# Optimization experiments

Hardware: AMD Instinct MI355X
Metric: run time of the kernel (lower is better)

Reference implementation:

```python
import jax, jax.numpy as jnp
import numpy as np

N, E, R = 50000, 500000, 3
IN, HID, OUT = 128, 128, 128
NEG_SLOPE = 0.2


def setup_inputs() -> dict:
    key = jax.random.key(0)
    ks = jax.random.split(key, 16)
    g = lambda i, shape: jax.random.normal(ks[i], shape, jnp.float32) * 0.1
    return {
        "x": jax.random.normal(ks[0], (N, IN), jnp.float32),
        "edge_index": jax.random.randint(ks[1], (2, E), 0, N, jnp.int32),
        "edge_type": jax.random.randint(ks[2], (E,), 0, R, jnp.int32),
        "edge_attr": jax.random.normal(ks[3], (E, 1), jnp.float32),
        # conv1 params (RGATConv: per-relation weight, q/k/e attention vectors, edge lin, bias)
        "w1": g(4, (R, IN, HID)), "q1": g(5, (HID, 1)), "k1": g(6, (HID, 1)),
        "le1": g(7, (1, HID)), "e1": g(8, (HID, 1)), "b1": jnp.zeros((HID,), jnp.float32),
        # conv2 params
        "w2": g(9, (R, HID, OUT)), "q2": g(10, (OUT, 1)), "k2": g(11, (OUT, 1)),
        "le2": g(12, (1, OUT)), "e2": g(13, (OUT, 1)), "b2": jnp.zeros((OUT,), jnp.float32),
    }


def _rgat_conv(x, src, dst, edge_type, edge_attr, w, q, k, le, e, b):
    """PyG RGATConv: heads=1, dim=1, additive-self-attention, across-relation softmax."""
    n = x.shape[0]
    # Per-relation linear at node level (equiv. to per-edge bmm with w[edge_type])
    xw = jnp.einsum('ni,rio->rno', x, w)            # [R, N, C]
    x_j = xw[edge_type, src]                          # [E, C] transformed source feats
    x_i = xw[edge_type, dst]                          # [E, C] transformed target feats
    # additive attention logits: q(x_i) + k(x_j) + e(lin_edge(edge_attr))
    alpha = x_i @ q + x_j @ k + (edge_attr @ le) @ e  # [E, 1]
    alpha = jax.nn.leaky_relu(alpha, negative_slope=NEG_SLOPE)
    # across-relation softmax over incoming edges of each target node
    amax = jax.ops.segment_max(alpha, dst, num_segments=n)
    amax = jnp.where(jnp.isfinite(amax), amax, 0.0)   # empty segments -> 0
    ex = jnp.exp(alpha - amax[dst])
    denom = jax.ops.segment_sum(ex, dst, num_segments=n)
    alpha = ex / (denom[dst] + 1e-16)
    # weighted scatter-add aggregation, then bias (concat=True, heads=1)
    out = jax.ops.segment_sum(alpha * x_j, dst, num_segments=n)  # [N, C]
    return out + b


def reference(x, edge_index, edge_type, edge_attr,
              w1, q1, k1, le1, e1, b1,
              w2, q2, k2, le2, e2, b2):
    src, dst = edge_index[0], edge_index[1]
    h = jax.nn.relu(_rgat_conv(x, src, dst, edge_type, edge_attr, w1, q1, k1, le1, e1, b1))
    return _rgat_conv(h, src, dst, edge_type, edge_attr, w2, q2, k2, le2, e2, b2)
```

## Files before the change

kernel.cpp:

```cpp
#include <hip/hip_runtime.h>
#include <hip/hip_bf16.h>
#include <math.h>

typedef __bf16 bf16x8 __attribute__((ext_vector_type(8)));
typedef float f32x4 __attribute__((ext_vector_type(4)));

#define CDIM 128

__global__ void sentinel_kernel(float* outf) {
  if (threadIdx.x == 0) outf[0] = 12345.0f;
}

__global__ __launch_bounds__(256) void prep_hist_kernel(
    const float* __restrict__ w1, const float* __restrict__ w2,
    __hip_bfloat16* __restrict__ wt,
    const float* __restrict__ le1, const float* __restrict__ e1,
    const float* __restrict__ le2, const float* __restrict__ e2,
    float* __restrict__ outc, const int* __restrict__ dstv,
    int* __restrict__ deg, int perW, int E) {
  const int b = blockIdx.x;
  const int tid = threadIdx.x;
  if (b < 48) {
    int t = b * 256 + tid;
    if (t >= perW * 2) return;
    const float* w = (t < perW) ? w1 : w2;
    int tt = (t < perW) ? t : t - perW;
    int r = tt >> 11;
    int rem = tt & 2047;
    int kb = rem >> 7;
    int o = rem & 127;
    const float* wr = w + ((size_t)r << 14);
    union { __hip_bfloat16 h[8]; int4 v; } u;
#pragma unroll
    for (int j = 0; j < 8; ++j)
      u.h[j] = __float2bfloat16(wr[(size_t)(kb * 8 + j) * CDIM + o]);
    *reinterpret_cast<int4*>(wt + (size_t)t * 8) = u.v;
  } else if (b == 48) {
    if (tid < 64) {
      float v1 = le1[tid] * e1[tid] + le1[tid + 64] * e1[tid + 64];
      float v2 = le2[tid] * e2[tid] + le2[tid + 64] * e2[tid + 64];
#pragma unroll
      for (int off = 32; off > 0; off >>= 1) {
        v1 += __shfl_xor(v1, off, 64);
        v2 += __shfl_xor(v2, off, 64);
      }
      if (tid == 0) { outc[0] = v1; outc[1] = v2; }
    }
  } else {
    int e = (b - 49) * 256 + tid;
    if (e < E) atomicAdd(&deg[dstv[e]], 1);
  }
}


__global__ __launch_bounds__(256) void scan1_kernel(const int* __restrict__ deg,
                                                    int* __restrict__ rowptr,
                                                    int* __restrict__ partials, int n) {
  __shared__ int sh[256];
  int t = threadIdx.x;
  int base = blockIdx.x * 1024;
  int idx = base + t * 4;
  int v[4]; int s = 0;
#pragma unroll
  for (int j = 0; j < 4; ++j) { v[j] = (idx + j < n) ? deg[idx + j] : 0; s += v[j]; }
  sh[t] = s;
  __syncthreads();
  for (int off = 1; off < 256; off <<= 1) {
    int x = (t >= off) ? sh[t - off] : 0;
    __syncthreads();
    sh[t] += x;
    __syncthreads();
  }
  int excl = sh[t] - s;
  if (t == 255) partials[blockIdx.x] = sh[255];
  int run = excl;
#pragma unroll
  for (int j = 0; j < 4; ++j) {
    if (idx + j < n) rowptr[idx + j] = run;
    run += v[j];
  }
}

__global__ __launch_bounds__(256) void scan3_kernel(int* __restrict__ rowptr,
                                                    int* __restrict__ cursor,
                                                    const int* __restrict__ partials,
                                                    int nb, int n, int E) {
  __shared__ int spfx[64];
  int t = threadIdx.x;
  if (t < 64) {
    int pv = (t < nb) ? partials[t] : 0;
    int v = pv;
#pragma unroll
    for (int off = 1; off < 64; off <<= 1) {
      int u = __shfl_up(v, off, 64);
      if (t >= off) v += u;
    }
    spfx[t] = v - pv;
  }
  __syncthreads();
  int i = blockIdx.x * 256 + t;
  if (i < n) {
    int v = rowptr[i] + spfx[i >> 10];
    rowptr[i] = v;
    cursor[i] = v;
  } else if (i == n) {
    rowptr[n] = E;
  }
}

__device__ __forceinline__ void gemm_body(
    int tileb, const float* __restrict__ xin, const __hip_bfloat16* __restrict__ wt,
    const float* __restrict__ qv, const float* __restrict__ kv,
    __hip_bfloat16* __restrict__ xwout, float* __restrict__ sq,
    float* __restrict__ sk, int n, __hip_bfloat16* wlds, float* qls, float* kls) {
  const int base = tileb * 128;
  const int tid = threadIdx.x;
  const int wave = tid >> 6, lane = tid & 63;
  const int quad = lane >> 4, c16 = lane & 15;

  if (tid < 128) qls[tid] = qv[tid];
  else kls[tid - 128] = kv[tid - 128];

  bf16x8 zf;
#pragma unroll
  for (int j = 0; j < 8; ++j) zf[j] = (__bf16)0.0f;

  bf16x8 af[2][4];
#pragma unroll
  for (int h = 0; h < 2; ++h) {
    int m = base + wave * 32 + h * 16 + c16;
#pragma unroll
    for (int ks = 0; ks < 4; ++ks) {
      if (m < n) {
        const float* xp = xin + (size_t)m * CDIM + ks * 32 + quad * 8;
        f32x4 x0 = *reinterpret_cast<const f32x4*>(xp);
        f32x4 x1 = *reinterpret_cast<const f32x4*>(xp + 4);
        bf16x8 a;
#pragma unroll
        for (int j = 0; j < 4; ++j) { a[j] = (__bf16)x0[j]; a[4 + j] = (__bf16)x1[j]; }
        af[h][ks] = a;
      } else {
        af[h][ks] = zf;
      }
    }
  }

  for (int r = 0; r < 3; ++r) {
    if (r) __syncthreads();
    {
      const int4* src = reinterpret_cast<const int4*>(wt + ((size_t)r << 14));
      int4* dst = reinterpret_cast<int4*>(wlds);
#pragma unroll
      for (int i = 0; i < 8; ++i) dst[tid + i * 256] = src[tid + i * 256];
    }
    __syncthreads();

    f32x4 acc[2][8];
#pragma unroll
    for (int h = 0; h < 2; ++h)
#pragma unroll
      for (int ot = 0; ot < 8; ++ot) acc[h][ot] = (f32x4){0.f, 0.f, 0.f, 0.f};

#pragma unroll
    for (int ks = 0; ks < 4; ++ks) {
#pragma unroll
      for (int ot = 0; ot < 8; ++ot) {
        bf16x8 b = *reinterpret_cast<const bf16x8*>(
            &wlds[(((ks * 4 + quad) * 128) + ot * 16 + c16) * 8]);
        acc[0][ot] = __builtin_amdgcn_mfma_f32_16x16x32_bf16(b, af[0][ks], acc[0][ot], 0, 0, 0);
        acc[1][ot] = __builtin_amdgcn_mfma_f32_16x16x32_bf16(b, af[1][ks], acc[1][ot], 0, 0, 0);
      }
    }

#pragma unroll
    for (int h = 0; h < 2; ++h) {
      const int grow = base + wave * 32 + h * 16 + c16;
      const bool ok = grow < n;
      __hip_bfloat16* rp = xwout + (((size_t)r * n + grow) << 7) + quad * 4;
      float s_q = 0.f, s_k = 0.f;
#pragma unroll
      for (int ot = 0; ot < 8; ++ot) {
        f32x4 a = acc[h][ot];
        f32x4 q4 = *reinterpret_cast<const f32x4*>(&qls[ot * 16 + quad * 4]);
        f32x4 k4 = *reinterpret_cast<const f32x4*>(&kls[ot * 16 + quad * 4]);
        s_q += a[0] * q4[0] + a[1] * q4[1] + a[2] * q4[2] + a[3] * q4[3];
        s_k += a[0] * k4[0] + a[1] * k4[1] + a[2] * k4[2] + a[3] * k4[3];
        if (ok) {
          union { __hip_bfloat16 b4[4]; uint2 u; } pk;
#pragma unroll
          for (int t = 0; t < 4; ++t) pk.b4[t] = __float2bfloat16(a[t]);
          *reinterpret_cast<uint2*>(rp + ot * 16) = pk.u;
        }
      }
      s_q += __shfl_xor(s_q, 16, 64);
      s_q += __shfl_xor(s_q, 32, 64);
      s_k += __shfl_xor(s_k, 16, 64);
      s_k += __shfl_xor(s_k, 32, 64);
      if (quad == 0 && ok) {
        sq[(size_t)r * n + grow] = s_q;
        sk[(size_t)r * n + grow] = s_k;
      }
    }
  }
}

__global__ __launch_bounds__(256) void gemm_scatter_kernel(
    const float* __restrict__ xin, const __hip_bfloat16* __restrict__ wt,
    const float* __restrict__ qv, const float* __restrict__ kv,
    __hip_bfloat16* __restrict__ xwout, float* __restrict__ sq, float* __restrict__ sk,
    const int* __restrict__ srcv, const int* __restrict__ dstv,
    const int* __restrict__ etype, const float* __restrict__ eattr,
    int* __restrict__ cursor, int2* __restrict__ kattr,
    int NT, int n, int E) {
  __shared__ __hip_bfloat16 wlds[16 * 128 * 8];
  __shared__ float qls[128], kls[128];
  const int b = blockIdx.x;
  if (b < NT) {
    gemm_body(b, xin, wt, qv, kv, xwout, sq, sk, n, wlds, qls, kls);
  } else {
    int e = (b - NT) * 256 + threadIdx.x;
    if (e < E) {
      int p = atomicAdd(&cursor[dstv[e]], 1);
      kattr[p] = make_int2(etype[e] * n + srcv[e], __float_as_int(eattr[e]));
    }
  }
}

__global__ __launch_bounds__(256) void gemm_xw_kernel(
    const float* __restrict__ xin, const __hip_bfloat16* __restrict__ wt,
    const float* __restrict__ qv, const float* __restrict__ kv,
    __hip_bfloat16* __restrict__ xwout, float* __restrict__ sq, float* __restrict__ sk,
    int n) {
  __shared__ __hip_bfloat16 wlds[16 * 128 * 8];
  __shared__ float qls[128], kls[128];
  gemm_body(blockIdx.x, xin, wt, qv, kv, xwout, sq, sk, n, wlds, qls, kls);
}

__global__ __launch_bounds__(256) void aggregate_kernel(
    const int* __restrict__ rowptr, const int2* __restrict__ kattr,
    const float* __restrict__ sq, const float* __restrict__ sk,
    const __hip_bfloat16* __restrict__ xw, const float* __restrict__ bias,
    const float* __restrict__ cscal, float* __restrict__ out, int n, int do_relu) {
  const int wave = threadIdx.x >> 6, lane = threadIdx.x & 63;
  const int g = lane >> 4;
  const int sub = lane & 15;
  const int node = blockIdx.x * 16 + wave * 4 + g;
  if (node >= n) return;
  const float c = cscal[0];
  const int n2 = n * 2;

  const int start = rowptr[node];
  const int deg = rowptr[node + 1] - start;
  const float s0 = sq[node], s1 = sq[n + node], s2 = sq[n2 + node];

  float acc[8];
#pragma unroll
  for (int t = 0; t < 8; ++t) acc[t] = 0.f;
  float den = 0.f;

  for (int j0 = 0; j0 < deg; j0 += 4) {
    int2 ka[4];
#pragma unroll
    for (int t = 0; t < 4; ++t) {
      int idx = j0 + t;
      ka[t] = kattr[start + (idx < deg ? idx : 0)];
    }
    float w[4];
    bf16x8 f[4];
#pragma unroll
    for (int t = 0; t < 4; ++t) {
      int kk = ka[t].x;
      float sv = (kk >= n2) ? s2 : ((kk >= n) ? s1 : s0);
      float l = sv + sk[kk] + c * __int_as_float(ka[t].y);
      l = l > 0.f ? l : 0.2f * l;
      w[t] = (j0 + t < deg) ? __expf(l) : 0.f;
      f[t] = *reinterpret_cast<const bf16x8*>(xw + ((size_t)kk << 7) + sub * 8);
    }
#pragma unroll
    for (int t = 0; t < 8; ++t)
      acc[t] += w[0] * (float)f[0][t] + w[1] * (float)f[1][t] +
                w[2] * (float)f[2][t] + w[3] * (float)f[3][t];
    den += (w[0] + w[1]) + (w[2] + w[3]);
  }

  float inv = 1.0f / (den + 1e-16f);
  f32x4 b0 = *reinterpret_cast<const f32x4*>(bias + sub * 8);
  f32x4 b1 = *reinterpret_cast<const f32x4*>(bias + sub * 8 + 4);
  f32x4 o0, o1;
#pragma unroll
  for (int t = 0; t < 4; ++t) {
    o0[t] = acc[t] * inv + b0[t];
    o1[t] = acc[4 + t] * inv + b1[t];
  }
  if (do_relu) {
#pragma unroll
    for (int t = 0; t < 4; ++t) {
      o0[t] = fmaxf(o0[t], 0.f);
      o1[t] = fmaxf(o1[t], 0.f);
    }
  }
  float* op = out + (size_t)node * CDIM + sub * 8;
  *reinterpret_cast<f32x4*>(op) = o0;
  *reinterpret_cast<f32x4*>(op + 4) = o1;
}


extern "C" void kernel_launch(void* const* d_in, const int* in_sizes, int n_in,
                              void* d_out, int out_size, void* d_ws, size_t ws_size,
                              hipStream_t stream) {
  const float* x     = (const float*)d_in[0];
  const int*   eidx  = (const int*)d_in[1];
  const int*   etype = (const int*)d_in[2];
  const float* eattr = (const float*)d_in[3];
  const float* w1  = (const float*)d_in[4];
  const float* q1  = (const float*)d_in[5];
  const float* k1  = (const float*)d_in[6];
  const float* le1 = (const float*)d_in[7];
  const float* e1  = (const float*)d_in[8];
  const float* b1  = (const float*)d_in[9];
  const float* w2  = (const float*)d_in[10];
  const float* q2  = (const float*)d_in[11];
  const float* k2  = (const float*)d_in[12];
  const float* le2 = (const float*)d_in[13];
  const float* e2  = (const float*)d_in[14];
  const float* b2  = (const float*)d_in[15];

  const int N = in_sizes[0] / CDIM;
  const int E = in_sizes[2];
  const int R = in_sizes[4] / (CDIM * CDIM);
  const int* srcv = eidx;
  const int* dstv = eidx + E;

  char* p = (char*)d_ws;
  auto alloc = [&](size_t bytes) -> void* {
    void* q = (void*)p;
    p += (bytes + 255) & ~(size_t)255;
    return q;
  };
  float* sq       = (float*)alloc((size_t)R * N * 4);
  float* sk       = (float*)alloc((size_t)R * N * 4);
  int*   deg      = (int*)alloc((size_t)N * 4);
  int*   rowptr   = (int*)alloc((size_t)(N + 1) * 4);
  int*   cursor   = (int*)alloc((size_t)N * 4);
  int*   partials = (int*)alloc(4096);
  int2*  kattr    = (int2*)alloc((size_t)E * 8);
  __hip_bfloat16* wt = (__hip_bfloat16*)alloc((size_t)2 * R * CDIM * CDIM * 2);
  float* cscal    = (float*)alloc(256);
  __hip_bfloat16* xw = (__hip_bfloat16*)alloc((size_t)R * N * CDIM * 2);

  size_t needed = (size_t)(p - (char*)d_ws);
  if (needed > ws_size) {
    sentinel_kernel<<<1, 64, 0, stream>>>((float*)d_out);
    return;
  }

  float* outp = (float*)d_out;
  float* hbuf = outp;

  const int eg = (E + 255) / 256;
  const int nb = (N + 1023) / 1024;
  const int NT = (N + 127) / 128;
  const int nodes16 = (N + 15) / 16;
  const int perW = R * 2048;

  hipMemsetAsync(deg, 0, (size_t)N * 4, stream);

  prep_hist_kernel<<<49 + eg, 256, 0, stream>>>(w1, w2, wt, le1, e1, le2, e2,
                                                cscal, dstv, deg, perW, E);

  scan1_kernel<<<nb, 256, 0, stream>>>(deg, rowptr, partials, N);
  scan3_kernel<<<(N + 1 + 255) / 256, 256, 0, stream>>>(rowptr, cursor, partials, nb, N, E);

  gemm_scatter_kernel<<<NT + eg, 256, 0, stream>>>(x, wt, q1, k1, xw, sq, sk,
                                                   srcv, dstv, etype, eattr,
                                                   cursor, kattr, NT, N, E);

  aggregate_kernel<<<nodes16, 256, 0, stream>>>(rowptr, kattr, sq, sk, xw, b1,
                                                cscal + 0, hbuf, N, 1);

  gemm_xw_kernel<<<NT, 256, 0, stream>>>(hbuf, wt + (size_t)R * CDIM * CDIM,
                                         q2, k2, xw, sq, sk, N);

  aggregate_kernel<<<nodes16, 256, 0, stream>>>(rowptr, kattr, sq, sk, xw, b2,
                                                cscal + 1, outp, N, 0);
}
```

Measured before the change: 241.4 us.

## Aggregate raw features per relation segment before applying relation weights

Reorders each RGAT layer so it aggregates first and transforms second. Edges are bucketed by (relation, destination), and attention logits come from precomputed W·q and W·k vectors. Gathers then read a single bf16 copy of the node features instead of the three per-relation transformed copies. The per-relation aggregates, with their partial denominators, are fed into one accumulated MFMA GEMM that also applies normalisation, bias, ReLU and the next layer's score projections. The aim is to shrink the random-gather working set and remove the separate per-relation xW materialisation. The cost is writing and reading 3N×128 bf16 aggregates, three times as many short segments, and unnormalised sums stored in bf16.

```diff
diff --git a/kernel.cpp b/kernel.cpp
--- a/kernel.cpp
+++ b/kernel.cpp
@@ -14,10 +14,13 @@
 __global__ __launch_bounds__(256) void prep_hist_kernel(
     const float* __restrict__ w1, const float* __restrict__ w2,
     __hip_bfloat16* __restrict__ wt,
+    const float* __restrict__ q1, const float* __restrict__ k1v,
+    const float* __restrict__ q2, const float* __restrict__ k2v,
     const float* __restrict__ le1, const float* __restrict__ e1,
     const float* __restrict__ le2, const float* __restrict__ e2,
-    float* __restrict__ outc, const int* __restrict__ dstv,
-    int* __restrict__ deg, int perW, int E) {
+    float* __restrict__ outc, float* __restrict__ wqk,
+    const int* __restrict__ dstv, const int* __restrict__ etype,
+    int* __restrict__ deg3, int perW, int n, int E) {
   const int b = blockIdx.x;
   const int tid = threadIdx.x;
   if (b < 48) {
@@ -46,23 +49,50 @@
       }
       if (tid == 0) { outc[0] = v1; outc[1] = v2; }
     }
+    for (int idx = tid; idx < 384; idx += 256) {
+      int r = idx >> 7, k = idx & 127;
+      const float* w1r = w1 + ((size_t)r << 14) + (size_t)k * 128;
+      const float* w2r = w2 + ((size_t)r << 14) + (size_t)k * 128;
+      float dq1 = 0.f, dk1 = 0.f, dq2 = 0.f, dk2 = 0.f;
+      for (int j = 0; j < 128; ++j) {
+        float a1 = w1r[j], a2 = w2r[j];
+        dq1 += a1 * q1[j];
+        dk1 += a1 * k1v[j];
+        dq2 += a2 * q2[j];
+        dk2 += a2 * k2v[j];
+      }
+      wqk[idx] = dq1;
+      wqk[384 + idx] = dk1;
+      wqk[768 + idx] = dq2;
+      wqk[1152 + idx] = dk2;
+    }
   } else {
-    int e = (b - 49) * 256 + tid;
-    if (e < E) atomicAdd(&deg[dstv[e]], 1);
-  }
-}
-
-
-__global__ __launch_bounds__(256) void scan1_kernel(const int* __restrict__ deg,
-                                                    int* __restrict__ rowptr,
-                                                    int* __restrict__ partials, int n) {
+    int e0 = (b - 49) * 1024 + tid * 4;
+    if (e0 + 3 < E) {
+      int4 d4 = *reinterpret_cast<const int4*>(&dstv[e0]);
+      int4 t4 = *reinterpret_cast<const int4*>(&etype[e0]);
+      atomicAdd(&deg3[t4.x * n + d4.x], 1);
+      atomicAdd(&deg3[t4.y * n + d4.y], 1);
+      atomicAdd(&deg3[t4.z * n + d4.z], 1);
+      atomicAdd(&deg3[t4.w * n + d4.w], 1);
+    } else {
+      for (int t = 0; t < 4; ++t) {
+        int e = e0 + t;
+        if (e < E) atomicAdd(&deg3[etype[e] * n + dstv[e]], 1);
+      }
+    }
+  }
+}
+
+__global__ __launch_bounds__(256) void scan1_kernel(const int* __restrict__ deg3,
+                                                    int* __restrict__ rowptr3,
+                                                    int* __restrict__ partials, int m3) {
   __shared__ int sh[256];
   int t = threadIdx.x;
-  int base = blockIdx.x * 1024;
-  int idx = base + t * 4;
-  int v[4]; int s = 0;
-#pragma unroll
-  for (int j = 0; j < 4; ++j) { v[j] = (idx + j < n) ? deg[idx + j] : 0; s += v[j]; }
+  int idx = blockIdx.x * 4096 + t * 16;
+  int v[16]; int s = 0;
+#pragma unroll
+  for (int j = 0; j < 16; ++j) { v[j] = (idx + j < m3) ? deg3[idx + j] : 0; s += v[j]; }
   sh[t] = s;
   __syncthreads();
   for (int off = 1; off < 256; off <<= 1) {
@@ -75,16 +105,16 @@
   if (t == 255) partials[blockIdx.x] = sh[255];
   int run = excl;
 #pragma unroll
-  for (int j = 0; j < 4; ++j) {
-    if (idx + j < n) rowptr[idx + j] = run;
+  for (int j = 0; j < 16; ++j) {
+    if (idx + j < m3) rowptr3[idx + j] = run;
     run += v[j];
   }
 }
 
-__global__ __launch_bounds__(256) void scan3_kernel(int* __restrict__ rowptr,
-                                                    int* __restrict__ cursor,
+__global__ __launch_bounds__(256) void scan3_kernel(int* __restrict__ rowptr3,
+                                                    int* __restrict__ cursor3,
                                                     const int* __restrict__ partials,
-                                                    int nb, int n, int E) {
+                                                    int nb, int m3, int E) {
   __shared__ int spfx[64];
   int t = threadIdx.x;
   if (t < 64) {
@@ -99,51 +129,171 @@
   }
   __syncthreads();
   int i = blockIdx.x * 256 + t;
-  if (i < n) {
-    int v = rowptr[i] + spfx[i >> 10];
-    rowptr[i] = v;
-    cursor[i] = v;
-  } else if (i == n) {
-    rowptr[n] = E;
-  }
-}
-
-__device__ __forceinline__ void gemm_body(
-    int tileb, const float* __restrict__ xin, const __hip_bfloat16* __restrict__ wt,
-    const float* __restrict__ qv, const float* __restrict__ kv,
-    __hip_bfloat16* __restrict__ xwout, float* __restrict__ sq,
-    float* __restrict__ sk, int n, __hip_bfloat16* wlds, float* qls, float* kls) {
-  const int base = tileb * 128;
+  if (i < m3) {
+    int v = rowptr3[i] + spfx[i >> 12];
+    rowptr3[i] = v;
+    cursor3[i] = v;
+  } else if (i == m3) {
+    rowptr3[m3] = E;
+  }
+}
+
+__global__ __launch_bounds__(256) void sqskxb_scatter_kernel(
+    const float* __restrict__ x, const float* __restrict__ wqk,
+    __hip_bfloat16* __restrict__ xb, float* __restrict__ sq1, float* __restrict__ sk1,
+    const int* __restrict__ srcv, const int* __restrict__ dstv,
+    const int* __restrict__ etype, const float* __restrict__ eattr,
+    int* __restrict__ cursor3, int2* __restrict__ kattr,
+    int NX, int n, int E) {
+  __shared__ float wls[768];
+  const int b = blockIdx.x;
+  const int tid = threadIdx.x;
+  if (b < NX) {
+    for (int i = tid; i < 768; i += 256) wls[i] = wqk[i];
+    __syncthreads();
+    const int row = b * 128 + (tid >> 1);
+    const int half = tid & 1;
+    if (row >= n) return;
+    const float* xp = x + (size_t)row * CDIM + half * 64;
+    __hip_bfloat16* xbp = xb + (size_t)row * CDIM + half * 64;
+    float a0 = 0.f, a1 = 0.f, a2 = 0.f, a3 = 0.f, a4 = 0.f, a5 = 0.f;
+#pragma unroll
+    for (int i = 0; i < 16; ++i) {
+      f32x4 v = *reinterpret_cast<const f32x4*>(xp + i * 4);
+      union { __hip_bfloat16 h[4]; uint2 u; } pk;
+#pragma unroll
+      for (int j = 0; j < 4; ++j) pk.h[j] = __float2bfloat16(v[j]);
+      *reinterpret_cast<uint2*>(xbp + i * 4) = pk.u;
+      const int cb = half * 64 + i * 4;
+#pragma unroll
+      for (int j = 0; j < 4; ++j) {
+        float xv = v[j];
+        a0 += xv * wls[cb + j];
+        a1 += xv * wls[128 + cb + j];
+        a2 += xv * wls[256 + cb + j];
+        a3 += xv * wls[384 + cb + j];
+        a4 += xv * wls[512 + cb + j];
+        a5 += xv * wls[640 + cb + j];
+      }
+    }
+    a0 += __shfl_xor(a0, 1, 64);
+    a1 += __shfl_xor(a1, 1, 64);
+    a2 += __shfl_xor(a2, 1, 64);
+    a3 += __shfl_xor(a3, 1, 64);
+    a4 += __shfl_xor(a4, 1, 64);
+    a5 += __shfl_xor(a5, 1, 64);
+    if (half == 0) {
+      sq1[row] = a0; sq1[n + row] = a1; sq1[2 * n + row] = a2;
+      sk1[row] = a3; sk1[n + row] = a4; sk1[2 * n + row] = a5;
+    }
+  } else {
+    int e0 = (b - NX) * 1024 + tid * 4;
+    if (e0 + 3 < E) {
+      int4 s4 = *reinterpret_cast<const int4*>(&srcv[e0]);
+      int4 d4 = *reinterpret_cast<const int4*>(&dstv[e0]);
+      int4 t4 = *reinterpret_cast<const int4*>(&etype[e0]);
+      float4 a4v = *reinterpret_cast<const float4*>(&eattr[e0]);
+      int p0 = atomicAdd(&cursor3[t4.x * n + d4.x], 1);
+      kattr[p0] = make_int2(s4.x, __float_as_int(a4v.x));
+      int p1 = atomicAdd(&cursor3[t4.y * n + d4.y], 1);
+      kattr[p1] = make_int2(s4.y, __float_as_int(a4v.y));
+      int p2 = atomicAdd(&cursor3[t4.z * n + d4.z], 1);
+      kattr[p2] = make_int2(s4.z, __float_as_int(a4v.z));
+      int p3 = atomicAdd(&cursor3[t4.w * n + d4.w], 1);
+      kattr[p3] = make_int2(s4.w, __float_as_int(a4v.w));
+    } else {
+      for (int t = 0; t < 4; ++t) {
+        int e = e0 + t;
+        if (e < E) {
+          int p = atomicAdd(&cursor3[etype[e] * n + dstv[e]], 1);
+          kattr[p] = make_int2(srcv[e], __float_as_int(eattr[e]));
+        }
+      }
+    }
+  }
+}
+
+__global__ __launch_bounds__(256) void agg_seg_kernel(
+    const int* __restrict__ rowptr3, const int2* __restrict__ kattr,
+    const float* __restrict__ sq, const float* __restrict__ sk,
+    const __hip_bfloat16* __restrict__ feat, const float* __restrict__ cscal,
+    __hip_bfloat16* __restrict__ hagg, float* __restrict__ den, int n, int m3) {
+  const int wave = threadIdx.x >> 6, lane = threadIdx.x & 63;
+  const int g = lane >> 4;
+  const int sub = lane & 15;
+  const int seg = blockIdx.x * 16 + wave * 4 + g;
+  if (seg >= m3) return;
+  const float c = cscal[0];
+  const int r = (seg >= 2 * n) ? 2 : ((seg >= n) ? 1 : 0);
+  const float* skr = sk + (size_t)r * n;
+
+  const int start = rowptr3[seg];
+  const int len = rowptr3[seg + 1] - start;
+  const float sv = sq[seg];
+
+  float acc[8];
+#pragma unroll
+  for (int t = 0; t < 8; ++t) acc[t] = 0.f;
+  float dn = 0.f;
+
+  for (int j0 = 0; j0 < len; j0 += 4) {
+    int2 ka[4];
+#pragma unroll
+    for (int t = 0; t < 4; ++t) {
+      int idx = j0 + t;
+      ka[t] = kattr[start + (idx < len ? idx : 0)];
+    }
+    float w[4];
+    bf16x8 f[4];
+#pragma unroll
+    for (int t = 0; t < 4; ++t) {
+      int src = ka[t].x;
+      float l = sv + skr[src] + c * __int_as_float(ka[t].y);
+      l = l > 0.f ? l : 0.2f * l;
+      w[t] = (j0 + t < len) ? __expf(l) : 0.f;
+      f[t] = *reinterpret_cast<const bf16x8*>(feat + ((size_t)src << 7) + sub * 8);
+    }
+#pragma unroll
+    for (int t = 0; t < 8; ++t)
+      acc[t] += w[0] * (float)f[0][t] + w[1] * (float)f[1][t] +
+                w[2] * (float)f[2][t] + w[3] * (float)f[3][t];
+    dn += (w[0] + w[1]) + (w[2] + w[3]);
+  }
+
+  union { __hip_bfloat16 h[8]; int4 v; } pk;
+#pragma unroll
+  for (int t = 0; t < 8; ++t) pk.h[t] = __float2bfloat16(acc[t]);
+  *reinterpret_cast<int4*>(hagg + ((size_t)seg << 7) + sub * 8) = pk.v;
+  if (sub == 0) den[seg] = dn;
+}
+
+template <int FINAL>
+__global__ __launch_bounds__(256) void gemm_ho_kernel(
+    const __hip_bfloat16* __restrict__ hagg, const float* __restrict__ den,
+    const __hip_bfloat16* __restrict__ wt, const float* __restrict__ bias,
+    const float* __restrict__ wqk2,
+    __hip_bfloat16* __restrict__ hb, float* __restrict__ sq2, float* __restrict__ sk2,
+    float* __restrict__ outf, int n) {
+  __shared__ __hip_bfloat16 wlds[16 * 128 * 8];
+  __shared__ float w2ls[768];
+  const int base = blockIdx.x * 128;
   const int tid = threadIdx.x;
   const int wave = tid >> 6, lane = tid & 63;
   const int quad = lane >> 4, c16 = lane & 15;
 
-  if (tid < 128) qls[tid] = qv[tid];
-  else kls[tid - 128] = kv[tid - 128];
+  if (FINAL == 0) {
+    for (int i = tid; i < 768; i += 256) w2ls[i] = wqk2[i];
+  }
 
   bf16x8 zf;
 #pragma unroll
   for (int j = 0; j < 8; ++j) zf[j] = (__bf16)0.0f;
 
-  bf16x8 af[2][4];
-#pragma unroll
-  for (int h = 0; h < 2; ++h) {
-    int m = base + wave * 32 + h * 16 + c16;
-#pragma unroll
-    for (int ks = 0; ks < 4; ++ks) {
-      if (m < n) {
-        const float* xp = xin + (size_t)m * CDIM + ks * 32 + quad * 8;
-        f32x4 x0 = *reinterpret_cast<const f32x4*>(xp);
-        f32x4 x1 = *reinterpret_cast<const f32x4*>(xp + 4);
-        bf16x8 a;
-#pragma unroll
-        for (int j = 0; j < 4; ++j) { a[j] = (__bf16)x0[j]; a[4 + j] = (__bf16)x1[j]; }
-        af[h][ks] = a;
-      } else {
-        af[h][ks] = zf;
-      }
-    }
-  }
+  f32x4 acc[2][8];
+#pragma unroll
+  for (int h = 0; h < 2; ++h)
+#pragma unroll
+    for (int ot = 0; ot < 8; ++ot) acc[h][ot] = (f32x4){0.f, 0.f, 0.f, 0.f};
 
   for (int r = 0; r < 3; ++r) {
     if (r) __syncthreads();
@@ -153,155 +303,86 @@
 #pragma unroll
       for (int i = 0; i < 8; ++i) dst[tid + i * 256] = src[tid + i * 256];
     }
+    bf16x8 af[2][4];
+#pragma unroll
+    for (int h = 0; h < 2; ++h) {
+      int m = base + wave * 32 + h * 16 + c16;
+#pragma unroll
+      for (int ks = 0; ks < 4; ++ks) {
+        af[h][ks] = (m < n)
+            ? *reinterpret_cast<const bf16x8*>(
+                  hagg + (((size_t)r * n + m) << 7) + ks * 32 + quad * 8)
+            : zf;
+      }
+    }
     __syncthreads();
 
-    f32x4 acc[2][8];
-#pragma unroll
-    for (int h = 0; h < 2; ++h)
-#pragma unroll
-      for (int ot = 0; ot < 8; ++ot) acc[h][ot] = (f32x4){0.f, 0.f, 0.f, 0.f};
-
 #pragma unroll
     for (int ks = 0; ks < 4; ++ks) {
 #pragma unroll
       for (int ot = 0; ot < 8; ++ot) {
-        bf16x8 b = *reinterpret_cast<const bf16x8*>(
+        bf16x8 bfrag = *reinterpret_cast<const bf16x8*>(
             &wlds[(((ks * 4 + quad) * 128) + ot * 16 + c16) * 8]);
-        acc[0][ot] = __builtin_amdgcn_mfma_f32_16x16x32_bf16(b, af[0][ks], acc[0][ot], 0, 0, 0);
-        acc[1][ot] = __builtin_amdgcn_mfma_f32_16x16x32_bf16(b, af[1][ks], acc[1][ot], 0, 0, 0);
-      }
-    }
-
-#pragma unroll
-    for (int h = 0; h < 2; ++h) {
-      const int grow = base + wave * 32 + h * 16 + c16;
-      const bool ok = grow < n;
-      __hip_bfloat16* rp = xwout + (((size_t)r * n + grow) << 7) + quad * 4;
-      float s_q = 0.f, s_k = 0.f;
+        acc[0][ot] = __builtin_amdgcn_mfma_f32_16x16x32_bf16(bfrag, af[0][ks], acc[0][ot], 0, 0, 0);
+        acc[1][ot] = __builtin_amdgcn_mfma_f32_16x16x32_bf16(bfrag, af[1][ks], acc[1][ot], 0, 0, 0);
+      }
+    }
+  }
+
+#pragma unroll
+  for (int h = 0; h < 2; ++h) {
+    const int grow = base + wave * 32 + h * 16 + c16;
+    const bool ok = grow < n;
+    float dtot = ok ? (den[grow] + den[n + grow] + den[2 * n + grow]) : 1.f;
+    float inv = 1.0f / (dtot + 1e-16f);
+    if (FINAL == 0) {
+      float s6[6];
+#pragma unroll
+      for (int j = 0; j < 6; ++j) s6[j] = 0.f;
 #pragma unroll
       for (int ot = 0; ot < 8; ++ot) {
+        const int col = ot * 16 + quad * 4;
+        f32x4 bv = *reinterpret_cast<const f32x4*>(bias + col);
         f32x4 a = acc[h][ot];
-        f32x4 q4 = *reinterpret_cast<const f32x4*>(&qls[ot * 16 + quad * 4]);
-        f32x4 k4 = *reinterpret_cast<const f32x4*>(&kls[ot * 16 + quad * 4]);
-        s_q += a[0] * q4[0] + a[1] * q4[1] + a[2] * q4[2] + a[3] * q4[3];
-        s_k += a[0] * k4[0] + a[1] * k4[1] + a[2] * k4[2] + a[3] * k4[3];
-        if (ok) {
-          union { __hip_bfloat16 b4[4]; uint2 u; } pk;
-#pragma unroll
-          for (int t = 0; t < 4; ++t) pk.b4[t] = __float2bfloat16(a[t]);
-          *reinterpret_cast<uint2*>(rp + ot * 16) = pk.u;
+        union { __hip_bfloat16 hh[4]; uint2 u; } pk;
+#pragma unroll
+        for (int j = 0; j < 4; ++j) {
+          float v = fmaxf(a[j] * inv + bv[j], 0.f);
+          pk.hh[j] = __float2bfloat16(v);
+          s6[0] += v * w2ls[col + j];
+          s6[1] += v * w2ls[128 + col + j];
+          s6[2] += v * w2ls[256 + col + j];
+          s6[3] += v * w2ls[384 + col + j];
+          s6[4] += v * w2ls[512 + col + j];
+          s6[5] += v * w2ls[640 + col + j];
         }
-      }
-      s_q += __shfl_xor(s_q, 16, 64);
-      s_q += __shfl_xor(s_q, 32, 64);
-      s_k += __shfl_xor(s_k, 16, 64);
-      s_k += __shfl_xor(s_k, 32, 64);
+        if (ok)
+          *reinterpret_cast<uint2*>(hb + ((size_t)grow << 7) + col) = pk.u;
+      }
+#pragma unroll
+      for (int j = 0; j < 6; ++j) {
+        s6[j] += __shfl_xor(s6[j], 16, 64);
+        s6[j] += __shfl_xor(s6[j], 32, 64);
+      }
       if (quad == 0 && ok) {
-        sq[(size_t)r * n + grow] = s_q;
-        sk[(size_t)r * n + grow] = s_k;
-      }
-    }
-  }
-}
-
-__global__ __launch_bounds__(256) void gemm_scatter_kernel(
-    const float* __restrict__ xin, const __hip_bfloat16* __restrict__ wt,
-    const float* __restrict__ qv, const float* __restrict__ kv,
-    __hip_bfloat16* __restrict__ xwout, float* __restrict__ sq, float* __restrict__ sk,
-    const int* __restrict__ srcv, const int* __restrict__ dstv,
-    const int* __restrict__ etype, const float* __restrict__ eattr,
-    int* __restrict__ cursor, int2* __restrict__ kattr,
-    int NT, int n, int E) {
-  __shared__ __hip_bfloat16 wlds[16 * 128 * 8];
-  __shared__ float qls[128], kls[128];
-  const int b = blockIdx.x;
-  if (b < NT) {
-    gemm_body(b, xin, wt, qv, kv, xwout, sq, sk, n, wlds, qls, kls);
-  } else {
-    int e = (b - NT) * 256 + threadIdx.x;
-    if (e < E) {
-      int p = atomicAdd(&cursor[dstv[e]], 1);
-      kattr[p] = make_int2(etype[e] * n + srcv[e], __float_as_int(eattr[e]));
-    }
-  }
-}
-
-__global__ __launch_bounds__(256) void gemm_xw_kernel(
-    const float* __restrict__ xin, const __hip_bfloat16* __restrict__ wt,
-    const float* __restrict__ qv, const float* __restrict__ kv,
-    __hip_bfloat16* __restrict__ xwout, float* __restrict__ sq, float* __restrict__ sk,
-    int n) {
-  __shared__ __hip_bfloat16 wlds[16 * 128 * 8];
-  __shared__ float qls[128], kls[128];
-  gemm_body(blockIdx.x, xin, wt, qv, kv, xwout, sq, sk, n, wlds, qls, kls);
-}
-
-__global__ __launch_bounds__(256) void aggregate_kernel(
-    const int* __restrict__ rowptr, const int2* __restrict__ kattr,
-    const float* __restrict__ sq, const float* __restrict__ sk,
-    const __hip_bfloat16* __restrict__ xw, const float* __restrict__ bias,
-    const float* __restrict__ cscal, float* __restrict__ out, int n, int do_relu) {
-  const int wave = threadIdx.x >> 6, lane = threadIdx.x & 63;
-  const int g = lane >> 4;
-  const int sub = lane & 15;
-  const int node = blockIdx.x * 16 + wave * 4 + g;
-  if (node >= n) return;
-  const float c = cscal[0];
-  const int n2 = n * 2;
-
-  const int start = rowptr[node];
-  const int deg = rowptr[node + 1] - start;
-  const float s0 = sq[node], s1 = sq[n + node], s2 = sq[n2 + node];
-
-  float acc[8];
-#pragma unroll
-  for (int t = 0; t < 8; ++t) acc[t] = 0.f;
-  float den = 0.f;
-
-  for (int j0 = 0; j0 < deg; j0 += 4) {
-    int2 ka[4];
-#pragma unroll
-    for (int t = 0; t < 4; ++t) {
-      int idx = j0 + t;
-      ka[t] = kattr[start + (idx < deg ? idx : 0)];
-    }
-    float w[4];
-    bf16x8 f[4];
-#pragma unroll
-    for (int t = 0; t < 4; ++t) {
-      int kk = ka[t].x;
-      float sv = (kk >= n2) ? s2 : ((kk >= n) ? s1 : s0);
-      float l = sv + sk[kk] + c * __int_as_float(ka[t].y);
-      l = l > 0.f ? l : 0.2f * l;
-      w[t] = (j0 + t < deg) ? __expf(l) : 0.f;
-      f[t] = *reinterpret_cast<const bf16x8*>(xw + ((size_t)kk << 7) + sub * 8);
-    }
-#pragma unroll
-    for (int t = 0; t < 8; ++t)
-      acc[t] += w[0] * (float)f[0][t] + w[1] * (float)f[1][t] +
-                w[2] * (float)f[2][t] + w[3] * (float)f[3][t];
-    den += (w[0] + w[1]) + (w[2] + w[3]);
-  }
-
-  float inv = 1.0f / (den + 1e-16f);
-  f32x4 b0 = *reinterpret_cast<const f32x4*>(bias + sub * 8);
-  f32x4 b1 = *reinterpret_cast<const f32x4*>(bias + sub * 8 + 4);
-  f32x4 o0, o1;
-#pragma unroll
-  for (int t = 0; t < 4; ++t) {
-    o0[t] = acc[t] * inv + b0[t];
-    o1[t] = acc[4 + t] * inv + b1[t];
-  }
-  if (do_relu) {
-#pragma unroll
-    for (int t = 0; t < 4; ++t) {
-      o0[t] = fmaxf(o0[t], 0.f);
-      o1[t] = fmaxf(o1[t], 0.f);
-    }
-  }
-  float* op = out + (size_t)node * CDIM + sub * 8;
-  *reinterpret_cast<f32x4*>(op) = o0;
-  *reinterpret_cast<f32x4*>(op + 4) = o1;
+        sq2[grow] = s6[0]; sq2[n + grow] = s6[1]; sq2[2 * n + grow] = s6[2];
+        sk2[grow] = s6[3]; sk2[n + grow] = s6[4]; sk2[2 * n + grow] = s6[5];
+      }
+    } else {
+      if (ok) {
+#pragma unroll
+        for (int ot = 0; ot < 8; ++ot) {
+          const int col = ot * 16 + quad * 4;
+          f32x4 bv = *reinterpret_cast<const f32x4*>(bias + col);
+          f32x4 a = acc[h][ot];
+          f32x4 o;
+#pragma unroll
+          for (int j = 0; j < 4; ++j) o[j] = a[j] * inv + bv[j];
+          *reinterpret_cast<f32x4*>(outf + (size_t)grow * CDIM + col) = o;
+        }
+      }
+    }
+  }
 }
 
 
@@ -328,6 +409,7 @@
   const int N = in_sizes[0] / CDIM;
   const int E = in_sizes[2];
   const int R = in_sizes[4] / (CDIM * CDIM);
+  const int M3 = R * N;
   const int* srcv = eidx;
   const int* dstv = eidx + E;
 
@@ -337,16 +419,24 @@
     p += (bytes + 255) & ~(size_t)255;
     return q;
   };
-  float* sq       = (float*)alloc((size_t)R * N * 4);
-  float* sk       = (float*)alloc((size_t)R * N * 4);
-  int*   deg      = (int*)alloc((size_t)N * 4);
-  int*   rowptr   = (int*)alloc((size_t)(N + 1) * 4);
-  int*   cursor   = (int*)alloc((size_t)N * 4);
+  float* sq1      = (float*)alloc((size_t)M3 * 4);
+  float* sk1      = (float*)alloc((size_t)M3 * 4);
+  float* sq2      = (float*)alloc((size_t)M3 * 4);
+  float* sk2      = (float*)alloc((size_t)M3 * 4);
+  int*   deg3     = (int*)alloc((size_t)M3 * 4);
+  int*   rowptr3  = (int*)alloc((size_t)(M3 + 1) * 4);
+  int*   cursor3  = (int*)alloc((size_t)M3 * 4);
   int*   partials = (int*)alloc(4096);
   int2*  kattr    = (int2*)alloc((size_t)E * 8);
   __hip_bfloat16* wt = (__hip_bfloat16*)alloc((size_t)2 * R * CDIM * CDIM * 2);
   float* cscal    = (float*)alloc(256);
-  __hip_bfloat16* xw = (__hip_bfloat16*)alloc((size_t)R * N * CDIM * 2);
+  float* wqk      = (float*)alloc(1536 * 4);
+  __hip_bfloat16* xb    = (__hip_bfloat16*)alloc((size_t)N * CDIM * 2);
+  __hip_bfloat16* hb    = (__hip_bfloat16*)alloc((size_t)N * CDIM * 2);
+  __hip_bfloat16* hagg1 = (__hip_bfloat16*)alloc((size_t)M3 * CDIM * 2);
+  __hip_bfloat16* hagg2 = (__hip_bfloat16*)alloc((size_t)M3 * CDIM * 2);
+  float* den1     = (float*)alloc((size_t)M3 * 4);
+  float* den2     = (float*)alloc((size_t)M3 * 4);
 
   size_t needed = (size_t)(p - (char*)d_ws);
   if (needed > ws_size) {
@@ -355,32 +445,38 @@
   }
 
   float* outp = (float*)d_out;
-  float* hbuf = outp;
-
-  const int eg = (E + 255) / 256;
-  const int nb = (N + 1023) / 1024;
-  const int NT = (N + 127) / 128;
-  const int nodes16 = (N + 15) / 16;
+
+  const int eg4 = (E + 1023) / 1024;
+  const int nb3 = (M3 + 4095) / 4096;
+  const int NX = (N + 127) / 128;
+  const int NA = (M3 + 15) / 16;
   const int perW = R * 2048;
 
-  hipMemsetAsync(deg, 0, (size_t)N * 4, stream);
-
-  prep_hist_kernel<<<49 + eg, 256, 0, stream>>>(w1, w2, wt, le1, e1, le2, e2,
-                                                cscal, dstv, deg, perW, E);
-
-  scan1_kernel<<<nb, 256, 0, stream>>>(deg, rowptr, partials, N);
-  scan3_kernel<<<(N + 1 + 255) / 256, 256, 0, stream>>>(rowptr, cursor, partials, nb, N, E);
-
-  gemm_scatter_kernel<<<NT + eg, 256, 0, stream>>>(x, wt, q1, k1, xw, sq, sk,
-                                                   srcv, dstv, etype, eattr,
-                                                   cursor, kattr, NT, N, E);
-
-  aggregate_kernel<<<nodes16, 256, 0, stream>>>(rowptr, kattr, sq, sk, xw, b1,
-                                                cscal + 0, hbuf, N, 1);
-
-  gemm_xw_kernel<<<NT, 256, 0, stream>>>(hbuf, wt + (size_t)R * CDIM * CDIM,
-                                         q2, k2, xw, sq, sk, N);
-
-  aggregate_kernel<<<nodes16, 256, 0, stream>>>(rowptr, kattr, sq, sk, xw, b2,
-                                                cscal + 1, outp, N, 0);
-}
+  hipMemsetAsync(deg3, 0, (size_t)M3 * 4, stream);
+
+  prep_hist_kernel<<<49 + eg4, 256, 0, stream>>>(w1, w2, wt, q1, k1, q2, k2,
+                                                 le1, e1, le2, e2, cscal, wqk,
+                                                 dstv, etype, deg3, perW, N, E);
+
+  scan1_kernel<<<nb3, 256, 0, stream>>>(deg3, rowptr3, partials, M3);
+  scan3_kernel<<<(M3 + 1 + 255) / 256, 256, 0, stream>>>(rowptr3, cursor3,
+                                                         partials, nb3, M3, E);
+
+  sqskxb_scatter_kernel<<<NX + eg4, 256, 0, stream>>>(x, wqk, xb, sq1, sk1,
+                                                      srcv, dstv, etype, eattr,
+                                                      cursor3, kattr, NX, N, E);
+
+  agg_seg_kernel<<<NA, 256, 0, stream>>>(rowptr3, kattr, sq1, sk1, xb,
+                                         cscal + 0, hagg1, den1, N, M3);
+
+  gemm_ho_kernel<0><<<NX, 256, 0, stream>>>(hagg1, den1, wt, b1, wqk + 768,
+                                            hb, sq2, sk2, nullptr, N);
+
+  agg_seg_kernel<<<NA, 256, 0, stream>>>(rowptr3, kattr, sq2, sk2, hb,
+                                         cscal + 1, hagg2, den2, N, M3);
+
+  gemm_ho_kernel<1><<<NX, 256, 0, stream>>>(hagg2, den2,
+                                            wt + (size_t)R * CDIM * CDIM, b2,
+                                            nullptr, nullptr, nullptr, nullptr,
+                                            outp, N);
+}
```

Result: slower. 283.0 us (+17.2%).
